# Performance work log

Hardware: AMD Instinct MI355X
Metric: run time of the kernel (lower is better)

The kernel has to match this reference:

```python
import jax, jax.numpy as jnp
import numpy as np

B, N, FIN, D, L, DF = 16, 768, 56, 140, 4, 128


def setup_inputs() -> dict:
    key = jax.random.key(0)
    ks = jax.random.split(key, 24)
    c_hs = jax.random.normal(ks[0], (B, N, FIN), jnp.float32)
    # receptor prefix length r, total atoms n (r < n <= N)
    r = jax.random.randint(ks[1], (B,), N // 4, N // 2)
    num_atoms = jax.random.randint(ks[2], (B,), (3 * N) // 4, N + 1).astype(jnp.int32)
    idx = jnp.arange(N)
    c_valid = (idx[None, :] < r[:, None]).astype(jnp.int32)
    # intra-molecule adjacency: sparse symmetric 0/1 with self loops
    a1 = (jax.random.uniform(ks[3], (B, N, N)) < 0.05).astype(jnp.float32)
    c_adjs1 = jnp.clip(jnp.maximum(a1, a1.transpose(0, 2, 1)) + jnp.eye(N, dtype=jnp.float32)[None], 0.0, 1.0)
    # cross distances in Angstroms
    d2 = jax.random.uniform(ks[4], (B, N, N), jnp.float32, 0.0, 20.0)
    c_adjs2 = 0.5 * (d2 + d2.transpose(0, 2, 1))
    s = 0.1
    params = dict(
        W_emb=s * jax.random.normal(ks[5], (FIN, D), jnp.float32),
        gat_W=s * jax.random.normal(ks[6], (L, D, D), jnp.float32),
        gat_Wb=jnp.zeros((L, D), jnp.float32),
        gat_A=s * jax.random.normal(ks[7], (L, D, D), jnp.float32),
        gat_gw=s * jax.random.normal(ks[8], (L, 2 * D, 1), jnp.float32),
        gat_gb=jnp.zeros((L, 1), jnp.float32),
        fc_w0=s * jax.random.normal(ks[9], (D, DF), jnp.float32),
        fc_b0=jnp.zeros((DF,), jnp.float32),
        fc_w1=s * jax.random.normal(ks[10], (DF, DF), jnp.float32),
        fc_b1=jnp.zeros((DF,), jnp.float32),
        fc_w2=s * jax.random.normal(ks[11], (DF, DF), jnp.float32),
        fc_b2=jnp.zeros((DF,), jnp.float32),
        fc_w3=s * jax.random.normal(ks[12], (DF, 1), jnp.float32),
        fc_b3=jnp.zeros((1,), jnp.float32),
        mu=jnp.array([4.0], jnp.float32),
        dev=jnp.array([1.0], jnp.float32),
    )
    return dict(c_hs=c_hs, c_adjs1=c_adjs1, c_adjs2=c_adjs2, c_valid=c_valid, num_atoms=num_atoms, **params)


def _formulate_adj2(adj2, c_valid, num_atoms, mu, dev):
    # vectorized version of the per-batch Python loop in Formulate_Adj2
    r = jnp.sum(c_valid > 0, axis=1)          # [B] receptor prefix length
    n = num_atoms                              # [B] total atoms
    i = jnp.arange(N)
    row_rec = i[None, :, None] < r[:, None, None]              # row < r
    col_lig = (i[None, None, :] >= r[:, None, None]) & (i[None, None, :] < n[:, None, None])
    maskA = row_rec & col_lig                  # [B,N,N] receptor-row x ligand-col block
    gauss = jnp.exp(-jnp.square(adj2 - mu) / dev)
    upd = jnp.where(adj2 <= 10.0, gauss, jnp.zeros_like(adj2))
    out = jnp.where(maskA, upd, adj2)
    out = jnp.where(maskA.transpose(0, 2, 1), out.transpose(0, 2, 1), out)  # symmetrize block
    return out


def _gat_gate(x, adj, W, Wb, A, gw, gb):
    h = x @ W + Wb                                             # [B,N,D]
    e = jnp.einsum('bjl,bkl->bjk', h @ A, h)                   # [B,N,N]
    e = e + e.transpose(0, 2, 1)
    att = jnp.where(adj > 0, e, jnp.float32(-9e15))
    att = jax.nn.softmax(att, axis=1)                          # NOTE: dim=1, as in torch code
    att = att * adj
    h_prime = jax.nn.relu(jnp.einsum('bij,bjk->bik', att, h))  # [B,N,D]
    coeff = jax.nn.sigmoid(jnp.concatenate([x, h_prime], -1) @ gw + gb)  # [B,N,1]
    return coeff * x + (1.0 - coeff) * h_prime


def reference(c_hs, c_adjs1, c_adjs2, c_valid, num_atoms, W_emb, gat_W, gat_Wb, gat_A, gat_gw, gat_gb,
              fc_w0, fc_b0, fc_w1, fc_b1, fc_w2, fc_b2, fc_w3, fc_b3, mu, dev):
    x = c_hs @ W_emb                                           # embede (no bias)
    adj2 = _formulate_adj2(c_adjs2, c_valid, num_atoms, mu, dev)
    for k in range(gat_W.shape[0]):                            # embede_graph (eval: dropout is identity)
        h1 = _gat_gate(x, c_adjs1, gat_W[k], gat_Wb[k], gat_A[k], gat_gw[k], gat_gb[k])
        h2 = _gat_gate(x, adj2, gat_W[k], gat_Wb[k], gat_A[k], gat_gw[k], gat_gb[k])
        x = h2 - h1
    # Get_Prediction: ragged sum pool over first num_atoms rows
    mask = (jnp.arange(N)[None, :] < num_atoms[:, None]).astype(x.dtype)
    pred = jnp.sum(x * mask[:, :, None], axis=1)               # [B,D]
    h = jax.nn.relu(pred @ fc_w0 + fc_b0)
    h = jax.nn.relu(h @ fc_w1 + fc_b1)
    h = jax.nn.relu(h @ fc_w2 + fc_b2)
    out = jax.nn.sigmoid(h @ fc_w3 + fc_b3)
    return out.reshape(-1)                                     # [B]
```

## Files before the change

kernel.cpp:

```cpp
#include <hip/hip_runtime.h>

constexpr int B   = 16;
constexpr int N   = 768;
constexpr int FIN = 56;
constexpr int D   = 140;
constexpr int L   = 4;
constexpr int DF  = 128;
constexpr int NN  = N * N;
constexpr int BND = B * N * D;
constexpr int BNN = B * NN;

constexpr int PROWS  = 16;
constexpr int NCHUNK = N / PROWS;

constexpr int NTILE = N / 64;
constexpr int NTRI  = NTILE * (NTILE + 1) / 2;

constexpr int JSPLIT = 4;
constexpr int JCH   = 32;

struct GatePtrs { float* g1[JSPLIT]; float* g2[JSPLIT]; };

template<int K>
__global__ __launch_bounds__(256) void k_linrb(const float* __restrict__ in,
                                               const float* __restrict__ W,
                                               const float* __restrict__ bias,
                                               float* __restrict__ out) {
    constexpr int NDG = D / 4;
    int idx = blockIdx.x * 256 + threadIdx.x;
    if (idx >= (B * N / 4) * NDG) return;
    int dt = idx % NDG;
    int rt = idx / NDG;
    int r0 = rt * 4, d = dt * 4;

    float acc[4][4];
    float b0 = 0.f, b1 = 0.f, b2 = 0.f, b3 = 0.f;
    if (bias) { b0 = bias[d]; b1 = bias[d + 1]; b2 = bias[d + 2]; b3 = bias[d + 3]; }
#pragma unroll
    for (int s = 0; s < 4; ++s) {
        acc[s][0] = b0; acc[s][1] = b1; acc[s][2] = b2; acc[s][3] = b3;
    }

#pragma unroll 2
    for (int k = 0; k < K; k += 4) {
        float4 wv[4];
#pragma unroll
        for (int kk = 0; kk < 4; ++kk)
            wv[kk] = *reinterpret_cast<const float4*>(&W[(size_t)(k + kk) * D + d]);
#pragma unroll
        for (int s = 0; s < 4; ++s) {
            float4 xv = *reinterpret_cast<const float4*>(&in[(size_t)(r0 + s) * K + k]);
            float xa[4] = {xv.x, xv.y, xv.z, xv.w};
#pragma unroll
            for (int kk = 0; kk < 4; ++kk) {
                acc[s][0] += xa[kk] * wv[kk].x;
                acc[s][1] += xa[kk] * wv[kk].y;
                acc[s][2] += xa[kk] * wv[kk].z;
                acc[s][3] += xa[kk] * wv[kk].w;
            }
        }
    }

#pragma unroll
    for (int s = 0; s < 4; ++s) {
        float4 v = {acc[s][0], acc[s][1], acc[s][2], acc[s][3]};
        *reinterpret_cast<float4*>(&out[(size_t)(r0 + s) * D + d]) = v;
    }
}

__global__ __launch_bounds__(256) void k_adj2(const float* __restrict__ a2,
                                              const int* __restrict__ valid,
                                              const int* __restrict__ natoms,
                                              const float* __restrict__ mu,
                                              const float* __restrict__ dev,
                                              float* __restrict__ out) {
    int idx = blockIdx.x * 256 + threadIdx.x;
    if (idx >= BNN) return;
    int b   = idx / NN;
    int rem = idx - b * NN;
    int i   = rem / N;
    int j   = rem - i * N;
    float a = a2[idx];
    int vi = valid[b * N + i];
    int vj = valid[b * N + j];
    int n  = natoms[b];
    bool mask = (vi && !vj && (j < n)) || (vj && !vi && (i < n));
    float dmu = a - mu[0];
    float g = (a <= 10.f) ? expf(-dmu * dmu / dev[0]) : 0.f;
    out[idx] = mask ? g : a;
}

__global__ __launch_bounds__(256) void k_e(const float* __restrict__ h,
                                           const float* __restrict__ hA,
                                           float* __restrict__ E) {
    int t = blockIdx.x;
    int b = blockIdx.y;
    int tj = 0, rem = t, rowlen = NTILE;
    while (rem >= rowlen) { rem -= rowlen; ++tj; --rowlen; }
    int tk = tj + rem;

    __shared__ float sJ[72][68];
    __shared__ float sK[72][68];
    int tid = threadIdx.x;
    int jg  = tid & 15;
    int kg  = tid >> 4;
    int j0 = tj * 64, k0 = tk * 64;
    const float* hb = h  + (size_t)b * N * D;
    const float* ab = hA + (size_t)b * N * D;

    float acc[4][4] = {};

    for (int r = 0; r < 4; ++r) {
        int ph = r >> 1;
        int c0 = (r & 1) ? 72 : 0;
        int kc = (r & 1) ? 68 : 72;
        int ncb = kc >> 2;
        const float* uS = ph ? hb : ab;
        const float* vS = ph ? ab : hb;
        if (r) __syncthreads();
        for (int idx = tid; idx < ncb * 16; idx += 256) {
            int cb = idx % ncb;
            int jb = (idx / ncb) * 4;
            int gc = c0 + cb * 4;
            float4 ru[4], rv[4];
#pragma unroll
            for (int s = 0; s < 4; ++s) {
                ru[s] = *reinterpret_cast<const float4*>(&uS[(size_t)(j0 + jb + s) * D + gc]);
                rv[s] = *reinterpret_cast<const float4*>(&vS[(size_t)(k0 + jb + s) * D + gc]);
            }
            float tu[4][4], tv[4][4];
#pragma unroll
            for (int s = 0; s < 4; ++s) {
                tu[s][0] = ru[s].x; tu[s][1] = ru[s].y; tu[s][2] = ru[s].z; tu[s][3] = ru[s].w;
                tv[s][0] = rv[s].x; tv[s][1] = rv[s].y; tv[s][2] = rv[s].z; tv[s][3] = rv[s].w;
            }
#pragma unroll
            for (int s = 0; s < 4; ++s) {
                float4 wu = {tu[0][s], tu[1][s], tu[2][s], tu[3][s]};
                float4 wv = {tv[0][s], tv[1][s], tv[2][s], tv[3][s]};
                *reinterpret_cast<float4*>(&sJ[cb * 4 + s][jb]) = wu;
                *reinterpret_cast<float4*>(&sK[cb * 4 + s][jb]) = wv;
            }
        }
        __syncthreads();
#pragma unroll 4
        for (int kk = 0; kk < kc; ++kk) {
            float4 ajv = *reinterpret_cast<const float4*>(&sJ[kk][jg * 4]);
            float4 akv = *reinterpret_cast<const float4*>(&sK[kk][kg * 4]);
            float aj[4] = {ajv.x, ajv.y, ajv.z, ajv.w};
            float ak[4] = {akv.x, akv.y, akv.z, akv.w};
#pragma unroll
            for (int i = 0; i < 4; ++i)
#pragma unroll
                for (int q = 0; q < 4; ++q) acc[i][q] += aj[i] * ak[q];
        }
    }

    float* Eb = E + (size_t)b * NN;
    int jb = j0 + jg * 4, kb = k0 + kg * 4;
#pragma unroll
    for (int i = 0; i < 4; ++i) {
        float4 v = {acc[i][0], acc[i][1], acc[i][2], acc[i][3]};
        *reinterpret_cast<float4*>(&Eb[(size_t)(jb + i) * N + kb]) = v;
    }
#pragma unroll
    for (int q = 0; q < 4; ++q) {
        float4 v = {acc[0][q], acc[1][q], acc[2][q], acc[3][q]};
        *reinterpret_cast<float4*>(&Eb[(size_t)(kb + q) * N + jb]) = v;
    }
}

__global__ __launch_bounds__(1024) void k_stats(const float* __restrict__ E,
                                                const float* __restrict__ a1,
                                                const float* __restrict__ a2,
                                                float* __restrict__ M1g, float* __restrict__ IS1g,
                                                float* __restrict__ M2g, float* __restrict__ IS2g) {
    int b    = blockIdx.y;
    int lane = threadIdx.x & 63;
    int js   = threadIdx.x >> 6;
    int k    = blockIdx.x * 64 + lane;
    const float* Eb = E  + (size_t)b * NN;
    const float* A1 = a1 + (size_t)b * NN;
    const float* A2 = a2 + (size_t)b * NN;

    float m1 = -3.0e38f, s1 = 0.f, m2 = -3.0e38f, s2 = 0.f;
    for (int j = js; j < N; j += 16) {
        float ev = Eb[(size_t)j * N + k];
        float v1 = A1[(size_t)j * N + k];
        float v2 = A2[(size_t)j * N + k];
        float x1 = (v1 > 0.f) ? ev : -9e15f;
        float x2 = (v2 > 0.f) ? ev : -9e15f;
        float n1 = fmaxf(m1, x1);
        s1 = s1 * __expf(m1 - n1) + __expf(x1 - n1);
        m1 = n1;
        float n2 = fmaxf(m2, x2);
        s2 = s2 * __expf(m2 - n2) + __expf(x2 - n2);
        m2 = n2;
    }
    __shared__ float sm1[16][64], ss1[16][64], sm2[16][64], ss2[16][64];
    sm1[js][lane] = m1; ss1[js][lane] = s1;
    sm2[js][lane] = m2; ss2[js][lane] = s2;
    __syncthreads();
    if (js == 0) {
        float M = sm1[0][lane], S = ss1[0][lane];
#pragma unroll
        for (int q = 1; q < 16; ++q) {
            float mq = sm1[q][lane], sq = ss1[q][lane];
            float nm = fmaxf(M, mq);
            S = S * __expf(M - nm) + sq * __expf(mq - nm);
            M = nm;
        }
        M1g[(size_t)b * N + k] = M;
        IS1g[(size_t)b * N + k] = 1.f / S;
        M = sm2[0][lane]; S = ss2[0][lane];
#pragma unroll
        for (int q = 1; q < 16; ++q) {
            float mq = sm2[q][lane], sq = ss2[q][lane];
            float nm = fmaxf(M, mq);
            S = S * __expf(M - nm) + sq * __expf(mq - nm);
            M = nm;
        }
        M2g[(size_t)b * N + k] = M;
        IS2g[(size_t)b * N + k] = 1.f / S;
    }
}

__global__ __launch_bounds__(192) void k_athf2(const float* __restrict__ E,
                                               const float* __restrict__ adj1,
                                               const float* __restrict__ adj2,
                                               const float* __restrict__ M1g,
                                               const float* __restrict__ IS1g,
                                               const float* __restrict__ M2g,
                                               const float* __restrict__ IS2g,
                                               const float* __restrict__ h,
                                               GatePtrs P) {
    int ti = blockIdx.x;
    int bz = blockIdx.y;
    int b  = bz >> 2;
    int js = bz & 3;
    __shared__ float sA1[JCH][68];
    __shared__ float sA2[JCH][68];
    __shared__ float sM1[192], sIS1[192], sM2[192], sIS2[192];
    int tid = threadIdx.x;
    int ig  = tid & 15;
    int dg  = tid >> 4;
    int i0  = ti * 64;
    const float* Eb = E    + (size_t)b * NN;
    const float* A1 = adj1 + (size_t)b * NN;
    const float* A2 = adj2 + (size_t)b * NN;
    const float* hb = h    + (size_t)b * N * D;
    int jbase = js * (N / JSPLIT);

    sM1[tid]  = M1g[(size_t)b * N + jbase + tid];
    sIS1[tid] = IS1g[(size_t)b * N + jbase + tid];
    sM2[tid]  = M2g[(size_t)b * N + jbase + tid];
    sIS2[tid] = IS2g[(size_t)b * N + jbase + tid];
    __syncthreads();

    float ac1[4][12] = {};
    float ac2[4][12] = {};

    for (int jt = 0; jt < (N / JSPLIT) / JCH; ++jt) {
        int j0 = jbase + jt * JCH;
        int jl = jt * JCH;
        if (jt) __syncthreads();
        if (tid < 128) {
            int jb4 = tid & 7, ib4 = tid >> 3;
            float4 ev[4], a1v[4], a2v[4];
#pragma unroll
            for (int s = 0; s < 4; ++s) {
                size_t off = (size_t)(i0 + ib4 * 4 + s) * N + (j0 + jb4 * 4);
                ev[s]  = *reinterpret_cast<const float4*>(&Eb[off]);
                a1v[s] = *reinterpret_cast<const float4*>(&A1[off]);
                a2v[s] = *reinterpret_cast<const float4*>(&A2[off]);
            }
            float mj1[4], is1[4], mj2[4], is2[4];
#pragma unroll
            for (int c = 0; c < 4; ++c) {
                mj1[c] = sM1[jl + jb4 * 4 + c];
                is1[c] = sIS1[jl + jb4 * 4 + c];
                mj2[c] = sM2[jl + jb4 * 4 + c];
                is2[c] = sIS2[jl + jb4 * 4 + c];
            }
            float t1[4][4], t2[4][4];
#pragma unroll
            for (int s = 0; s < 4; ++s) {
                float ea[4] = {ev[s].x, ev[s].y, ev[s].z, ev[s].w};
                float b1[4] = {a1v[s].x, a1v[s].y, a1v[s].z, a1v[s].w};
                float b2[4] = {a2v[s].x, a2v[s].y, a2v[s].z, a2v[s].w};
#pragma unroll
                for (int c = 0; c < 4; ++c) {
                    float x1 = (b1[c] > 0.f) ? ea[c] : -9e15f;
                    float x2 = (b2[c] > 0.f) ? ea[c] : -9e15f;
                    t1[s][c] = __expf(x1 - mj1[c]) * is1[c] * b1[c];
                    t2[s][c] = __expf(x2 - mj2[c]) * is2[c] * b2[c];
                }
            }
#pragma unroll
            for (int c = 0; c < 4; ++c) {
                int row = jb4 * 4 + c;
                int col = (ib4 * 4) ^ (((row >> 2) & 7) << 2);
                float4 w1 = {t1[0][c], t1[1][c], t1[2][c], t1[3][c]};
                float4 w2 = {t2[0][c], t2[1][c], t2[2][c], t2[3][c]};
                *reinterpret_cast<float4*>(&sA1[row][col]) = w1;
                *reinterpret_cast<float4*>(&sA2[row][col]) = w2;
            }
        }
        __syncthreads();
#pragma unroll 2
        for (int kk = 0; kk < JCH; ++kk) {
            int col = (ig * 4) ^ (((kk >> 2) & 7) << 2);
            float4 a4 = *reinterpret_cast<const float4*>(&sA1[kk][col]);
            float4 b4 = *reinterpret_cast<const float4*>(&sA2[kk][col]);
            const float* hrow = hb + (size_t)(j0 + kk) * D + dg * 12;
            float4 h0 = *reinterpret_cast<const float4*>(&hrow[0]);
            float4 h1 = *reinterpret_cast<const float4*>(&hrow[4]);
            float4 h2 = *reinterpret_cast<const float4*>(&hrow[8]);
            float ai[4]  = {a4.x, a4.y, a4.z, a4.w};
            float bi[4]  = {b4.x, b4.y, b4.z, b4.w};
            float hd[12] = {h0.x, h0.y, h0.z, h0.w,
                            h1.x, h1.y, h1.z, h1.w,
                            h2.x, h2.y, h2.z, h2.w};
#pragma unroll
            for (int i = 0; i < 4; ++i)
#pragma unroll
                for (int q = 0; q < 12; ++q) {
                    ac1[i][q] += ai[i] * hd[q];
                    ac2[i][q] += bi[i] * hd[q];
                }
        }
    }

    float* d1 = P.g1[js] + (size_t)b * N * D;
    float* d2 = P.g2[js] + (size_t)b * N * D;
#pragma unroll
    for (int s = 0; s < 4; ++s) {
        int row = i0 + ig * 4 + s;
#pragma unroll
        for (int t = 0; t < 3; ++t) {
            int cc = dg * 12 + t * 4;
            if (cc < D) {
                float4 v1 = {ac1[s][t * 4], ac1[s][t * 4 + 1],
                             ac1[s][t * 4 + 2], ac1[s][t * 4 + 3]};
                float4 v2 = {ac2[s][t * 4], ac2[s][t * 4 + 1],
                             ac2[s][t * 4 + 2], ac2[s][t * 4 + 3]};
                *reinterpret_cast<float4*>(&d1[(size_t)row * D + cc]) = v1;
                *reinterpret_cast<float4*>(&d2[(size_t)row * D + cc]) = v2;
            }
        }
    }
}

__global__ __launch_bounds__(64) void k_gate2(float* __restrict__ x,
                                              GatePtrs P,
                                              const float* __restrict__ gw,
                                              const float* __restrict__ gb) {
    int row  = blockIdx.x;
    int lane = threadIdx.x;
    float* xr = x + (size_t)row * D;
    const float* q1[JSPLIT];
    const float* q2[JSPLIT];
#pragma unroll
    for (int e = 0; e < JSPLIT; ++e) {
        q1[e] = P.g1[e] + (size_t)row * D;
        q2[e] = P.g2[e] + (size_t)row * D;
    }
    float xv[3], h1v[3], h2v[3];
    float p1 = 0.f, p2 = 0.f;
#pragma unroll
    for (int q = 0; q < 3; ++q) {
        int d = lane + q * 64;
        xv[q] = 0.f; h1v[q] = 0.f; h2v[q] = 0.f;
        if (d < D) {
            xv[q] = xr[d];
            float s1 = q1[0][d];
#pragma unroll
            for (int e = 1; e < JSPLIT; ++e) s1 += q1[e][d];
            h1v[q] = fmaxf(s1, 0.f);
            float s2 = q2[0][d];
#pragma unroll
            for (int e = 1; e < JSPLIT; ++e) s2 += q2[e][d];
            h2v[q] = fmaxf(s2, 0.f);
            p1 += xv[q] * gw[d] + h1v[q] * gw[D + d];
            p2 += xv[q] * gw[d] + h2v[q] * gw[D + d];
        }
    }
#pragma unroll
    for (int off = 32; off; off >>= 1) {
        p1 += __shfl_xor(p1, off);
        p2 += __shfl_xor(p2, off);
    }
    float c1 = 1.f / (1.f + __expf(-(p1 + gb[0])));
    float c2 = 1.f / (1.f + __expf(-(p2 + gb[0])));
#pragma unroll
    for (int q = 0; q < 3; ++q) {
        int d = lane + q * 64;
        if (d < D) {
            float v1 = c1 * xv[q] + (1.f - c1) * h1v[q];
            float v2 = c2 * xv[q] + (1.f - c2) * h2v[q];
            xr[d] = v2 - v1;
        }
    }
}

__global__ __launch_bounds__(256) void k_pool(const float* __restrict__ x,
                                              const int* __restrict__ natoms,
                                              float* __restrict__ part) {
    int c = blockIdx.x;
    int b = blockIdx.y;
    int tid = threadIdx.x;
    if (tid >= D) return;
    int n  = natoms[b];
    int r0 = c * PROWS;
    int r1 = min(r0 + PROWS, n);
    const float* xb = x + (size_t)b * N * D;
    float acc = 0.f;
    for (int r = r0; r < r1; ++r) acc += xb[(size_t)r * D + tid];
    part[((size_t)b * NCHUNK + c) * D + tid] = acc;
}

__global__ __launch_bounds__(256) void k_final(const float* __restrict__ part,
                                               const float* __restrict__ w0, const float* __restrict__ b0,
                                               const float* __restrict__ w1, const float* __restrict__ b1,
                                               const float* __restrict__ w2, const float* __restrict__ b2,
                                               const float* __restrict__ w3, const float* __restrict__ b3,
                                               float* __restrict__ out) {
    int b   = blockIdx.x;
    int tid = threadIdx.x;
    __shared__ float pred[D];
    __shared__ float h0[DF], h1[DF], h2[DF];
    if (tid < D) {
        float acc = 0.f;
        const float* pb = part + (size_t)b * NCHUNK * D;
#pragma unroll 8
        for (int c = 0; c < NCHUNK; ++c) acc += pb[(size_t)c * D + tid];
        pred[tid] = acc;
    }
    __syncthreads();
    if (tid < DF) {
        float acc = b0[tid];
#pragma unroll 4
        for (int i = 0; i < D; ++i) acc += pred[i] * w0[i * DF + tid];
        h0[tid] = fmaxf(acc, 0.f);
    }
    __syncthreads();
    if (tid < DF) {
        float acc = b1[tid];
#pragma unroll 4
        for (int i = 0; i < DF; ++i) acc += h0[i] * w1[i * DF + tid];
        h1[tid] = fmaxf(acc, 0.f);
    }
    __syncthreads();
    if (tid < DF) {
        float acc = b2[tid];
#pragma unroll 4
        for (int i = 0; i < DF; ++i) acc += h1[i] * w2[i * DF + tid];
        h2[tid] = fmaxf(acc, 0.f);
    }
    __syncthreads();
    if (tid == 0) {
        float acc = b3[0];
        for (int i = 0; i < DF; ++i) acc += h2[i] * w3[i];
        out[b] = 1.f / (1.f + expf(-acc));
    }
}

extern "C" void kernel_launch(void* const* d_in, const int* in_sizes, int n_in,
                              void* d_out, int out_size, void* d_ws, size_t ws_size,
                              hipStream_t stream) {
    const float* c_hs  = (const float*)d_in[0];
    const float* adj1  = (const float*)d_in[1];
    const float* c_a2  = (const float*)d_in[2];
    const int*   valid = (const int*)d_in[3];
    const int*   nat   = (const int*)d_in[4];
    const float* Wemb  = (const float*)d_in[5];
    const float* gatW  = (const float*)d_in[6];
    const float* gatWb = (const float*)d_in[7];
    const float* gatA  = (const float*)d_in[8];
    const float* gatgw = (const float*)d_in[9];
    const float* gatgb = (const float*)d_in[10];
    const float* w0 = (const float*)d_in[11];
    const float* b0 = (const float*)d_in[12];
    const float* w1 = (const float*)d_in[13];
    const float* b1 = (const float*)d_in[14];
    const float* w2 = (const float*)d_in[15];
    const float* b2 = (const float*)d_in[16];
    const float* w3 = (const float*)d_in[17];
    const float* b3 = (const float*)d_in[18];
    const float* mu  = (const float*)d_in[19];
    const float* dev = (const float*)d_in[20];
    float* out = (float*)d_out;

    float* ws    = (float*)d_ws;
    float* adj2f = ws;
    float* Ebuf  = adj2f + BNN;
    float* ATTws = Ebuf + BNN;
    float* x     = ATTws + BNN;
    float* h     = x + BND;
    float* hA    = h + BND;
    float* hp    = hA + BND;
    float* g1    = hp + BND;
    float* pC    = g1 + BND;
    float* pD    = pC + BND;
    float* p4 = ATTws;
    float* p5 = ATTws + (size_t)1 * BND;
    float* p6 = ATTws + (size_t)2 * BND;
    float* p7 = ATTws + (size_t)3 * BND;
    float* M1  = ATTws + (size_t)4 * BND;
    float* IS1 = M1 + (size_t)B * N;
    float* M2  = IS1 + (size_t)B * N;
    float* IS2 = M2 + (size_t)B * N;
    GatePtrs P;
    P.g1[0] = hp; P.g1[1] = hA; P.g1[2] = g1; P.g1[3] = pC;
    P.g2[0] = p4; P.g2[1] = p5; P.g2[2] = p6; P.g2[3] = p7;
    float* part  = Ebuf;

    constexpr int LIN_GRID = (B * N / 4) * (D / 4) / 256;

    k_linrb<FIN><<<LIN_GRID, 256, 0, stream>>>(c_hs, Wemb, nullptr, x);
    k_adj2<<<(BNN + 255) / 256, 256, 0, stream>>>(c_a2, valid, nat, mu, dev, adj2f);

    for (int l = 0; l < L; ++l) {
        const float* Wl  = gatW + (size_t)l * D * D;
        const float* Wbl = gatWb + (size_t)l * D;
        const float* Al  = gatA + (size_t)l * D * D;
        const float* gwl = gatgw + (size_t)l * 2 * D;
        const float* gbl = gatgb + l;

        k_linrb<D><<<LIN_GRID, 256, 0, stream>>>(x, Wl, Wbl, h);
        k_linrb<D><<<LIN_GRID, 256, 0, stream>>>(h, Al, nullptr, hA);
        k_e<<<dim3(NTRI, B), 256, 0, stream>>>(h, hA, Ebuf);

        k_stats<<<dim3(N / 64, B), 1024, 0, stream>>>(Ebuf, adj1, adj2f,
                                                      M1, IS1, M2, IS2);

        k_athf2<<<dim3(NTILE, B * JSPLIT), 192, 0, stream>>>(Ebuf, adj1, adj2f,
                                                             M1, IS1, M2, IS2,
                                                             h, P);
        k_gate2<<<B * N, 64, 0, stream>>>(x, P, gwl, gbl);
    }

    k_pool<<<dim3(NCHUNK, B), 256, 0, stream>>>(x, nat, part);
    k_final<<<B, 256, 0, stream>>>(part, w0, b0, w1, b1, w2, b2, w3, b3, out);
}
```

Measured before the change: 1.353 ms.

## Double-buffer attention tiles in k_athf2 to overlap global loads with FMA loop

Double-buffers the shared-memory attention tiles in the fused attention-times-h kernel. The global loads of E/adj1/adj2 for the next chunk are issued before the inner FMA loop, and the softmax-weighted tile is written into the other buffer afterwards, so there is one barrier per chunk instead of two. This is meant to hide global load latency behind compute, at the cost of 48 extra live float4 registers and double the LDS for the tiles, which may lower occupancy.

```diff
diff --git a/kernel.cpp b/kernel.cpp
--- a/kernel.cpp
+++ b/kernel.cpp
@@ -18,6 +18,7 @@
 
 constexpr int JSPLIT = 4;
 constexpr int JCH   = 32;
+constexpr int NCHK  = (N / JSPLIT) / JCH;
 
 struct GatePtrs { float* g1[JSPLIT]; float* g2[JSPLIT]; };
 
@@ -238,8 +239,8 @@
     int bz = blockIdx.y;
     int b  = bz >> 2;
     int js = bz & 3;
-    __shared__ float sA1[JCH][68];
-    __shared__ float sA2[JCH][68];
+    __shared__ float sA1[2][JCH][68];
+    __shared__ float sA2[2][JCH][68];
     __shared__ float sM1[192], sIS1[192], sM2[192], sIS2[192];
     int tid = threadIdx.x;
     int ig  = tid & 15;
@@ -257,30 +258,31 @@
     sIS2[tid] = IS2g[(size_t)b * N + jbase + tid];
     __syncthreads();
 
-    float ac1[4][12] = {};
-    float ac2[4][12] = {};
-
-    for (int jt = 0; jt < (N / JSPLIT) / JCH; ++jt) {
-        int j0 = jbase + jt * JCH;
-        int jl = jt * JCH;
-        if (jt) __syncthreads();
-        if (tid < 128) {
-            int jb4 = tid & 7, ib4 = tid >> 3;
-            float4 ev[4], a1v[4], a2v[4];
+    int  jb4 = tid & 7, ib4 = tid >> 3;
+    bool stg = (tid < 128);
+    float4 ev[4], a1v[4], a2v[4];
+
+    auto LOADC = [&](int jtn) {
+        if (stg && jtn < NCHK) {
+            int j0n = jbase + jtn * JCH;
 #pragma unroll
             for (int s = 0; s < 4; ++s) {
-                size_t off = (size_t)(i0 + ib4 * 4 + s) * N + (j0 + jb4 * 4);
+                size_t off = (size_t)(i0 + ib4 * 4 + s) * N + (j0n + jb4 * 4);
                 ev[s]  = *reinterpret_cast<const float4*>(&Eb[off]);
                 a1v[s] = *reinterpret_cast<const float4*>(&A1[off]);
                 a2v[s] = *reinterpret_cast<const float4*>(&A2[off]);
             }
+        }
+    };
+    auto WRITEC = [&](int jtn) {
+        if (stg && jtn < NCHK) {
+            int p = jtn & 1;
             float mj1[4], is1[4], mj2[4], is2[4];
 #pragma unroll
             for (int c = 0; c < 4; ++c) {
-                mj1[c] = sM1[jl + jb4 * 4 + c];
-                is1[c] = sIS1[jl + jb4 * 4 + c];
-                mj2[c] = sM2[jl + jb4 * 4 + c];
-                is2[c] = sIS2[jl + jb4 * 4 + c];
+                int jj = jtn * JCH + jb4 * 4 + c;
+                mj1[c] = sM1[jj]; is1[c] = sIS1[jj];
+                mj2[c] = sM2[jj]; is2[c] = sIS2[jj];
             }
             float t1[4][4], t2[4][4];
 #pragma unroll
@@ -302,16 +304,28 @@
                 int col = (ib4 * 4) ^ (((row >> 2) & 7) << 2);
                 float4 w1 = {t1[0][c], t1[1][c], t1[2][c], t1[3][c]};
                 float4 w2 = {t2[0][c], t2[1][c], t2[2][c], t2[3][c]};
-                *reinterpret_cast<float4*>(&sA1[row][col]) = w1;
-                *reinterpret_cast<float4*>(&sA2[row][col]) = w2;
-            }
-        }
-        __syncthreads();
+                *reinterpret_cast<float4*>(&sA1[p][row][col]) = w1;
+                *reinterpret_cast<float4*>(&sA2[p][row][col]) = w2;
+            }
+        }
+    };
+
+    float ac1[4][12] = {};
+    float ac2[4][12] = {};
+
+    LOADC(0);
+    WRITEC(0);
+    __syncthreads();
+
+    for (int jt = 0; jt < NCHK; ++jt) {
+        int p  = jt & 1;
+        int j0 = jbase + jt * JCH;
+        LOADC(jt + 1);
 #pragma unroll 2
         for (int kk = 0; kk < JCH; ++kk) {
             int col = (ig * 4) ^ (((kk >> 2) & 7) << 2);
-            float4 a4 = *reinterpret_cast<const float4*>(&sA1[kk][col]);
-            float4 b4 = *reinterpret_cast<const float4*>(&sA2[kk][col]);
+            float4 a4 = *reinterpret_cast<const float4*>(&sA1[p][kk][col]);
+            float4 b4 = *reinterpret_cast<const float4*>(&sA2[p][kk][col]);
             const float* hrow = hb + (size_t)(j0 + kk) * D + dg * 12;
             float4 h0 = *reinterpret_cast<const float4*>(&hrow[0]);
             float4 h1 = *reinterpret_cast<const float4*>(&hrow[4]);
@@ -329,6 +343,8 @@
                     ac2[i][q] += bi[i] * hd[q];
                 }
         }
+        WRITEC(jt + 1);
+        __syncthreads();
     }
 
     float* d1 = P.g1[js] + (size_t)b * N * D;
```

Measured after the change: 1.363 ms. About the same (+0.8%).
